# Kernel optimization log

Measured on AMD Instinct MI355X. Metric: run time of the kernel, lower is better.

Reference implementation:

```python
import jax, jax.numpy as jnp
import numpy as np
import math

B, S, H, NH, K = 1, 4096, 1024, 16, 32
HD = H // NH


def setup_inputs() -> dict:
    key = jax.random.key(0)
    ks = jax.random.split(key, 8)
    x = jax.random.normal(ks[0], (B, S, H), dtype=jnp.float32)
    # per-query top-K indices; make them causal (idx[q] <= q) so every row has >=1 valid key
    idx_raw = jax.random.randint(ks[1], (S, K), 0, S)
    idx = idx_raw % (jnp.arange(S)[:, None] + 1)
    valid = jnp.ones((S, K), dtype=bool)
    geo_bias = jax.random.normal(ks[2], (NH, S, K), dtype=jnp.float32)
    scale = 1.0 / math.sqrt(H)
    Wq = jax.random.normal(ks[3], (H, H), dtype=jnp.float32) * scale
    Wk = jax.random.normal(ks[4], (H, H), dtype=jnp.float32) * scale
    Wv = jax.random.normal(ks[5], (H, H), dtype=jnp.float32) * scale
    Wo = jax.random.normal(ks[6], (H, H), dtype=jnp.float32) * scale
    bo = jnp.zeros((H,), dtype=jnp.float32)
    return {"x": x, "idx": idx, "valid": valid, "geo_bias": geo_bias,
            "Wq": Wq, "Wk": Wk, "Wv": Wv, "Wo": Wo, "bo": bo}


def reference(x, idx, valid, geo_bias, Wq, Wk, Wv, Wo, bo):
    b, s, h = x.shape
    nh = geo_bias.shape[0]
    hd = h // nh
    kk = idx.shape[1]
    # projections -> [b, nh, s, hd]
    def proj(W):
        return (x @ W).reshape(b, s, nh, hd).transpose(0, 2, 1, 3)
    q, k, v = proj(Wq), proj(Wk), proj(Wv)
    # gather per-query selected keys/values: [b, nh, s, K, hd]
    k_sel = k[:, :, idx]
    v_sel = v[:, :, idx]
    # scores via elementwise mult + reduce over head_dim
    logits = jnp.einsum('bhsd,bhskd->bhsk', q, k_sel) / math.sqrt(hd)
    logits = logits + geo_bias[None]
    mask = valid & (idx <= jnp.arange(s)[:, None])  # [s, K]
    logits = jnp.where(mask[None, None], logits, jnp.float32(-1e30))
    attn = jax.nn.softmax(logits, axis=-1)
    out = jnp.einsum('bhsk,bhskd->bhsd', attn, v_sel)
    out = out.transpose(0, 2, 1, 3).reshape(b, s, h)
    return out @ Wo + bo
```

## Files before the change

kernel.cpp:

```cpp
#include <hip/hip_runtime.h>
#include <hip/hip_bf16.h>
#include <stdint.h>

typedef unsigned short u16;
typedef __attribute__((ext_vector_type(8))) short bf16x8;
typedef __attribute__((ext_vector_type(4))) float f32x4;
typedef __attribute__((ext_vector_type(2))) float f32x2;

typedef const __attribute__((address_space(1))) unsigned int* gptr_t;
typedef __attribute__((address_space(3))) unsigned int* lptr_t;

__device__ __forceinline__ u16 f2bf(float f) {
    unsigned int u;
    __builtin_memcpy(&u, &f, 4);
    u += 0x7FFFu + ((u >> 16) & 1u);
    return (u16)(u >> 16);
}
__device__ __forceinline__ float bflo(unsigned int u) {
    unsigned int x = u << 16; float f; __builtin_memcpy(&f, &x, 4); return f;
}
__device__ __forceinline__ float bfhi(unsigned int u) {
    unsigned int x = u & 0xFFFF0000u; float f; __builtin_memcpy(&f, &x, 4); return f;
}
__device__ __forceinline__ f32x2 upk(unsigned int u) {
    return (f32x2){bflo(u), bfhi(u)};
}

__global__ __launch_bounds__(256) void gemm_qkv(const u16* __restrict__ A,
                                                const u16* __restrict__ Bt,
                                                u16* __restrict__ C,
                                                int M, int N, int K) {
    __shared__ u16 S[4][4096];

    const int t    = threadIdx.x;
    const int lane = t & 63;
    const int wave = t >> 6;
    const int wm   = (wave >> 1) * 64;
    const int wn   = (wave & 1) * 64;
    const int m0   = blockIdx.y * 128;
    const int n0   = blockIdx.x * 128;

    const int r5   = t >> 2;
    const int pc   = t & 3;
    const int lc   = pc ^ ((r5 >> 1) & 3);

    const int quad = lane >> 4;
    const int l16  = lane & 15;
    const int swz  = (l16 >> 1) & 3;

    const u16* gabase = A  + (size_t)(m0 + r5) * K + lc * 8;
    const u16* gbbase = Bt + (size_t)(n0 + r5) * K + lc * 8;

    f32x4 acc[4][4];
#pragma unroll
    for (int i = 0; i < 4; i++)
#pragma unroll
        for (int j = 0; j < 4; j++) acc[i][j] = (f32x4){0.f, 0.f, 0.f, 0.f};

    const int NT = K >> 5;

#pragma unroll
    for (int p = 0; p < 2; p++) {
        __builtin_amdgcn_global_load_lds((gptr_t)(gabase + (size_t)(64 * p) * K),
                                         (lptr_t)(&S[0][t * 8 + p * 2048]), 16, 0, 0);
        __builtin_amdgcn_global_load_lds((gptr_t)(gbbase + (size_t)(64 * p) * K),
                                         (lptr_t)(&S[2][t * 8 + p * 2048]), 16, 0, 0);
    }
#pragma unroll
    for (int p = 0; p < 2; p++) {
        __builtin_amdgcn_global_load_lds((gptr_t)(gabase + (size_t)(64 * p) * K + 32),
                                         (lptr_t)(&S[1][t * 8 + p * 2048]), 16, 0, 0);
        __builtin_amdgcn_global_load_lds((gptr_t)(gbbase + (size_t)(64 * p) * K + 32),
                                         (lptr_t)(&S[3][t * 8 + p * 2048]), 16, 0, 0);
    }
    asm volatile("s_waitcnt vmcnt(4)");
    __builtin_amdgcn_sched_barrier(0);
    __builtin_amdgcn_s_barrier();

    for (int kt = 0; kt < NT; ++kt) {
        const int buf = kt & 1;

        bf16x8 af[4], bfg[4];
#pragma unroll
        for (int i = 0; i < 4; i++)
            af[i] = *(const bf16x8*)&S[buf][(wm + i * 16 + l16) * 32 + ((quad ^ swz) * 8)];
#pragma unroll
        for (int j = 0; j < 4; j++)
            bfg[j] = *(const bf16x8*)&S[2 + buf][(wn + j * 16 + l16) * 32 + ((quad ^ swz) * 8)];
        asm volatile("s_waitcnt lgkmcnt(0)");
        __builtin_amdgcn_sched_barrier(0);
        __builtin_amdgcn_s_barrier();

        if (kt + 2 < NT) {
            const int k0 = (kt + 2) * 32;
#pragma unroll
            for (int p = 0; p < 2; p++) {
                __builtin_amdgcn_global_load_lds(
                    (gptr_t)(gabase + (size_t)(64 * p) * K + k0),
                    (lptr_t)(&S[buf][t * 8 + p * 2048]), 16, 0, 0);
                __builtin_amdgcn_global_load_lds(
                    (gptr_t)(gbbase + (size_t)(64 * p) * K + k0),
                    (lptr_t)(&S[2 + buf][t * 8 + p * 2048]), 16, 0, 0);
            }
        }

#pragma unroll
        for (int i = 0; i < 4; i++)
#pragma unroll
            for (int j = 0; j < 4; j++)
                acc[i][j] = __builtin_amdgcn_mfma_f32_16x16x32_bf16(af[i], bfg[j], acc[i][j], 0, 0, 0);

        if (kt < NT - 2) {
            asm volatile("s_waitcnt vmcnt(4)");
            __builtin_amdgcn_sched_barrier(0);
            __builtin_amdgcn_s_barrier();
        } else if (kt == NT - 2) {
            asm volatile("s_waitcnt vmcnt(0)");
            __builtin_amdgcn_sched_barrier(0);
            __builtin_amdgcn_s_barrier();
        }
    }

    __syncthreads();

    u16* Cs = &S[0][0];
#pragma unroll
    for (int j = 0; j < 4; j++)
#pragma unroll
        for (int i = 0; i < 4; i++)
#pragma unroll
            for (int r = 0; r < 4; r++)
                Cs[(wm + i * 16 + quad * 4 + r) * 128 + wn + j * 16 + l16] = f2bf(acc[i][j][r]);
    __syncthreads();

#pragma unroll
    for (int p = 0; p < 8; p++) {
        const int row = p * 16 + (t >> 4);
        const int c8  = (t & 15) * 8;
        const uint4 v = *(const uint4*)&Cs[row * 128 + c8];
        *(uint4*)&C[(size_t)(m0 + row) * N + n0 + c8] = v;
    }
}

__global__ __launch_bounds__(256) void gemm_o(const u16* __restrict__ A,
                                              const u16* __restrict__ Bt,
                                              float* __restrict__ C,
                                              const float* __restrict__ bias,
                                              int M, int N, int K) {
    __shared__ u16 As[128 * 64];
    __shared__ u16 Bs[64 * 64];

    const int t    = threadIdx.x;
    const int lane = t & 63;
    const int wave = t >> 6;
    const int wm   = (wave >> 1) * 64;
    const int wn   = (wave & 1) * 32;
    const int m0   = blockIdx.y * 128;
    const int n0   = blockIdx.x * 64;

    const int r5   = t >> 3;
    const int pc   = t & 7;
    const int lc   = pc ^ (r5 & 7);

    const int quad = lane >> 4;
    const int l16  = lane & 15;
    const int sw   = l16 & 7;

    f32x4 acc[4][2];
#pragma unroll
    for (int i = 0; i < 4; i++)
#pragma unroll
        for (int j = 0; j < 2; j++) acc[i][j] = (f32x4){0.f, 0.f, 0.f, 0.f};

    for (int k0 = 0; k0 < K; k0 += 64) {
#pragma unroll
        for (int p = 0; p < 4; p++) {
            const u16* ga = A + (size_t)(m0 + r5 + 32 * p) * K + k0 + lc * 8;
            __builtin_amdgcn_global_load_lds((gptr_t)ga, (lptr_t)(&As[t * 8 + p * 2048]), 16, 0, 0);
        }
#pragma unroll
        for (int p = 0; p < 2; p++) {
            const u16* gb = Bt + (size_t)(n0 + r5 + 32 * p) * K + k0 + lc * 8;
            __builtin_amdgcn_global_load_lds((gptr_t)gb, (lptr_t)(&Bs[t * 8 + p * 2048]), 16, 0, 0);
        }
        __syncthreads();

#pragma unroll
        for (int k2 = 0; k2 < 2; k2++) {
            bf16x8 af[4], bfg[2];
#pragma unroll
            for (int i = 0; i < 4; i++)
                af[i] = *(const bf16x8*)&As[(wm + i * 16 + l16) * 64 + ((k2 * 4 + quad) ^ sw) * 8];
#pragma unroll
            for (int j = 0; j < 2; j++)
                bfg[j] = *(const bf16x8*)&Bs[(wn + j * 16 + l16) * 64 + ((k2 * 4 + quad) ^ sw) * 8];
#pragma unroll
            for (int i = 0; i < 4; i++)
#pragma unroll
                for (int j = 0; j < 2; j++)
                    acc[i][j] = __builtin_amdgcn_mfma_f32_16x16x32_bf16(af[i], bfg[j], acc[i][j], 0, 0, 0);
        }
        __syncthreads();
    }

#pragma unroll
    for (int j = 0; j < 2; j++) {
        const int n  = n0 + wn + j * 16 + l16;
        const float bv = bias ? bias[n] : 0.f;
#pragma unroll
        for (int i = 0; i < 4; i++) {
            const int mbase = m0 + wm + i * 16 + quad * 4;
#pragma unroll
            for (int r = 0; r < 4; r++)
                C[(size_t)(mbase + r) * N + n] = acc[i][j][r] + bv;
        }
    }
}

__global__ __launch_bounds__(256) void prep_k(const float* __restrict__ x,
                                              const float* __restrict__ W0,
                                              const float* __restrict__ W1,
                                              const float* __restrict__ W2,
                                              const float* __restrict__ W3,
                                              u16* __restrict__ x_bf,
                                              u16* __restrict__ Dqkv,
                                              u16* __restrict__ Do) {
    const int b = blockIdx.x;
    if (b < 4096) {
        const int i = b * 256 + threadIdx.x;
        const float4 v = ((const float4*)x)[i];
        u16 o[4] = {f2bf(v.x), f2bf(v.y), f2bf(v.z), f2bf(v.w)};
        *(uint64_t*)&x_bf[i * 4] = *(uint64_t*)o;
        return;
    }
    __shared__ u16 tile[32][33];
    const int bb  = b - 4096;
    const int z   = bb >> 10;
    const int t10 = bb & 1023;
    const int c0  = (t10 & 31) * 32;
    const int r0  = (t10 >> 5) * 32;
    const float* src = (z == 0) ? W0 : (z == 1) ? W1 : (z == 2) ? W2 : W3;
    u16* dst = (z < 3) ? (Dqkv + (size_t)z * 1024 * 1024) : Do;
    const int tx = threadIdx.x & 31;
    const int ty = threadIdx.x >> 5;
#pragma unroll
    for (int i = 0; i < 32; i += 8)
        tile[ty + i][tx] = f2bf(src[(size_t)(r0 + ty + i) * 1024 + c0 + tx]);
    __syncthreads();
#pragma unroll
    for (int i = 0; i < 32; i += 8)
        dst[(size_t)(c0 + ty + i) * 1024 + r0 + tx] = tile[tx][ty + i];
}

__global__ __launch_bounds__(256, 6) void attn_k(const u16* __restrict__ QKV,
                                                 const int* __restrict__ idx,
                                                 const float* __restrict__ geo,
                                                 u16* __restrict__ AO) {
    __shared__ float dot_lds[4 * 64];
    __shared__ float w_lds[4 * 64];

    const int t    = threadIdx.x;
    const int lane = t & 63;
    const int wave = t >> 6;
    const int b    = blockIdx.x;
    const int hp   = b & 7;
    const int s    = ((b >> 3) << 2) + wave;
    const int h0   = hp * 2;
    const int hsel = lane >> 5;
    const int kk   = lane & 31;
    const int g    = lane >> 3;
    const int c8   = lane & 7;

    const char* qb = (const char*)QKV;

    const float gv = geo[((size_t)(h0 + hsel) * 4096 + s) * 32 + kk];
    const int j    = idx[s * 32 + kk];
    const int joff = j * 6144;

    const uint4 qA = *(const uint4*)(qb + (size_t)s * 6144 + h0 * 128 + c8 * 16);
    const uint4 qB = *(const uint4*)(qb + (size_t)s * 6144 + h0 * 128 + 128 + c8 * 16);

    int jsrc0 = __shfl(j, (0 * 8 + g) & 31);
    int jsrc1 = __shfl(j, (1 * 8 + g) & 31);
    int jsrc2 = __shfl(j, (2 * 8 + g) & 31);
    int jsrc3 = __shfl(j, (3 * 8 + g) & 31);

    uint4 kreg[8];
#pragma unroll
    for (int i = 0; i < 8; i++) {
        const int jm = (i & 3) == 0 ? jsrc0 : (i & 3) == 1 ? jsrc1
                     : (i & 3) == 2 ? jsrc2 : jsrc3;
        kreg[i] = *(const uint4*)(qb + (size_t)(unsigned)(jm * 6144) + 2048 +
                                  (h0 + (i >> 2)) * 128 + c8 * 16);
    }
    __builtin_amdgcn_sched_barrier(0);

    const f32x2 qa0 = upk(qA.x), qa1 = upk(qA.y), qa2 = upk(qA.z), qa3 = upk(qA.w);
    const f32x2 qb0 = upk(qB.x), qb1 = upk(qB.y), qb2 = upk(qB.z), qb3 = upk(qB.w);

#pragma unroll
    for (int i = 0; i < 8; i++) {
        const int rh = i * 8 + g;
        f32x2 d2;
        if (i < 4) {
            d2  = upk(kreg[i].x) * qa0;
            d2 += upk(kreg[i].y) * qa1;
            d2 += upk(kreg[i].z) * qa2;
            d2 += upk(kreg[i].w) * qa3;
        } else {
            d2  = upk(kreg[i].x) * qb0;
            d2 += upk(kreg[i].y) * qb1;
            d2 += upk(kreg[i].z) * qb2;
            d2 += upk(kreg[i].w) * qb3;
        }
        float d = d2.x + d2.y;
        d += __shfl_xor(d, 1);
        d += __shfl_xor(d, 2);
        d += __shfl_xor(d, 4);
        if (c8 == 0) dot_lds[wave * 64 + rh] = d;
    }

    float lg2 = dot_lds[wave * 64 + lane] * 0.125f + gv;
    if (j > s) lg2 = -1e30f;
    lg2 = fminf(lg2, 80.f);

    const float p = __expf(lg2);
    float sum = p;
    sum += __shfl_xor(sum, 16);
    sum += __shfl_xor(sum, 8);
    sum += __shfl_xor(sum, 4);
    sum += __shfl_xor(sum, 2);
    sum += __shfl_xor(sum, 1);
    const float w = p / sum;
    w_lds[wave * 64 + lane] = w;

    const int half = lane >> 5;
    const int e8   = lane & 31;
    const int vconst = 4096 + h0 * 128 + 8 * e8;
    uint2 vreg[16];
#pragma unroll
    for (int i = 0; i < 16; i++) {
        const int jo = __shfl(joff, 2 * i + half);
        vreg[i] = *(const uint2*)(qb + (size_t)(unsigned)jo + vconst);
    }
    __builtin_amdgcn_sched_barrier(0);

    const int whead = (e8 >> 4) * 32;
    f32x2 a01a = (f32x2){0.f, 0.f}, a01b = (f32x2){0.f, 0.f};
    f32x2 a23a = (f32x2){0.f, 0.f}, a23b = (f32x2){0.f, 0.f};
#pragma unroll
    for (int i = 0; i < 16; i += 2) {
        const float w0 = w_lds[wave * 64 + whead + 2 * i + half];
        const float w1 = w_lds[wave * 64 + whead + 2 * (i + 1) + half];
        a01a += w0 * upk(vreg[i].x);
        a23a += w0 * upk(vreg[i].y);
        a01b += w1 * upk(vreg[i + 1].x);
        a23b += w1 * upk(vreg[i + 1].y);
    }
    f32x2 av01 = a01a + a01b;
    f32x2 av23 = a23a + a23b;
    av01.x += __shfl_xor(av01.x, 32);
    av01.y += __shfl_xor(av01.y, 32);
    av23.x += __shfl_xor(av23.x, 32);
    av23.y += __shfl_xor(av23.y, 32);
    if (lane < 32) {
        u16 o[4] = {f2bf(av01.x), f2bf(av01.y), f2bf(av23.x), f2bf(av23.y)};
        *(uint2*)&AO[(size_t)s * 1024 + h0 * 64 + 4 * lane] = *(uint2*)o;
    }
}

extern "C" void kernel_launch(void* const* d_in, const int* in_sizes, int n_in,
                              void* d_out, int out_size, void* d_ws, size_t ws_size,
                              hipStream_t stream) {
    const float* x   = (const float*)d_in[0];
    const int*   idx = (const int*)d_in[1];
    const float* geo = (const float*)d_in[3];
    const float* Wq  = (const float*)d_in[4];
    const float* Wk  = (const float*)d_in[5];
    const float* Wv  = (const float*)d_in[6];
    const float* Wo  = (const float*)d_in[7];
    const float* bo  = (const float*)d_in[8];
    float* out = (float*)d_out;

    u16* x_bf   = (u16*)d_ws;
    u16* wt_qkv = x_bf + (size_t)4096 * 1024;
    u16* wt_o   = wt_qkv + (size_t)3 * 1024 * 1024;
    u16* qkv    = wt_o + (size_t)1024 * 1024;
    u16* ao     = qkv + (size_t)4096 * 3072;

    const dim3 tb(256);
    prep_k<<<dim3(8192), tb, 0, stream>>>(x, Wq, Wk, Wv, Wo, x_bf, wt_qkv, wt_o);

    gemm_qkv<<<dim3(3072 / 128, 4096 / 128), tb, 0, stream>>>(
        x_bf, wt_qkv, qkv, 4096, 3072, 1024);
    attn_k<<<dim3(4096 * 8 / 4), tb, 0, stream>>>(qkv, idx, geo, ao);
    gemm_o<<<dim3(1024 / 64, 4096 / 128), tb, 0, stream>>>(
        ao, wt_o, out, bo, 4096, 1024, 1024);
}
```

Baseline: 182.0 us.

## Remap QK dot lanes to 4-lane groups and load V indices directly

```diff
diff --git a/kernel.cpp b/kernel.cpp
--- a/kernel.cpp
+++ b/kernel.cpp
@@ -268,56 +268,64 @@
     const int h0   = hp * 2;
     const int hsel = lane >> 5;
     const int kk   = lane & 31;
-    const int g    = lane >> 3;
-    const int c8   = lane & 7;
+    const int c4   = lane & 3;
+    const int g16  = lane >> 2;
 
     const char* qb = (const char*)QKV;
 
     const float gv = geo[((size_t)(h0 + hsel) * 4096 + s) * 32 + kk];
     const int j    = idx[s * 32 + kk];
-    const int joff = j * 6144;
-
-    const uint4 qA = *(const uint4*)(qb + (size_t)s * 6144 + h0 * 128 + c8 * 16);
-    const uint4 qB = *(const uint4*)(qb + (size_t)s * 6144 + h0 * 128 + 128 + c8 * 16);
-
-    int jsrc0 = __shfl(j, (0 * 8 + g) & 31);
-    int jsrc1 = __shfl(j, (1 * 8 + g) & 31);
-    int jsrc2 = __shfl(j, (2 * 8 + g) & 31);
-    int jsrc3 = __shfl(j, (3 * 8 + g) & 31);
-
-    uint4 kreg[8];
-#pragma unroll
-    for (int i = 0; i < 8; i++) {
-        const int jm = (i & 3) == 0 ? jsrc0 : (i & 3) == 1 ? jsrc1
-                     : (i & 3) == 2 ? jsrc2 : jsrc3;
-        kreg[i] = *(const uint4*)(qb + (size_t)(unsigned)(jm * 6144) + 2048 +
-                                  (h0 + (i >> 2)) * 128 + c8 * 16);
-    }
-    __builtin_amdgcn_sched_barrier(0);
-
-    const f32x2 qa0 = upk(qA.x), qa1 = upk(qA.y), qa2 = upk(qA.z), qa3 = upk(qA.w);
-    const f32x2 qb0 = upk(qB.x), qb1 = upk(qB.y), qb2 = upk(qB.z), qb3 = upk(qB.w);
-
-#pragma unroll
-    for (int i = 0; i < 8; i++) {
-        const int rh = i * 8 + g;
+
+    const int jA = idx[s * 32 + g16];
+    const int jB = idx[s * 32 + 16 + g16];
+
+    const int half = lane >> 5;
+    const uint4 jv0 = *(const uint4*)&idx[s * 32 + 16 * half + 0];
+    const uint4 jv1 = *(const uint4*)&idx[s * 32 + 16 * half + 4];
+    const uint4 jv2 = *(const uint4*)&idx[s * 32 + 16 * half + 8];
+    const uint4 jv3 = *(const uint4*)&idx[s * 32 + 16 * half + 12];
+    const int jvs[16] = {(int)jv0.x, (int)jv0.y, (int)jv0.z, (int)jv0.w,
+                         (int)jv1.x, (int)jv1.y, (int)jv1.z, (int)jv1.w,
+                         (int)jv2.x, (int)jv2.y, (int)jv2.z, (int)jv2.w,
+                         (int)jv3.x, (int)jv3.y, (int)jv3.z, (int)jv3.w};
+
+    const char* qrow = qb + (size_t)s * 6144 + h0 * 128;
+    const uint4 qA0 = *(const uint4*)(qrow + c4 * 16);
+    const uint4 qA1 = *(const uint4*)(qrow + 64 + c4 * 16);
+    const uint4 qB0 = *(const uint4*)(qrow + 128 + c4 * 16);
+    const uint4 qB1 = *(const uint4*)(qrow + 192 + c4 * 16);
+
+#pragma unroll
+    for (int i = 0; i < 4; i++) {
+        const int ji = (i & 1) ? jB : jA;
+        const char* kb = qb + (size_t)(unsigned)(ji * 6144) + 2048 +
+                         (h0 + (i >> 1)) * 128;
+        const uint4 k0 = *(const uint4*)(kb + c4 * 16);
+        const uint4 k1 = *(const uint4*)(kb + 64 + c4 * 16);
         f32x2 d2;
-        if (i < 4) {
-            d2  = upk(kreg[i].x) * qa0;
-            d2 += upk(kreg[i].y) * qa1;
-            d2 += upk(kreg[i].z) * qa2;
-            d2 += upk(kreg[i].w) * qa3;
+        if (i < 2) {
+            d2  = upk(k0.x) * upk(qA0.x);
+            d2 += upk(k0.y) * upk(qA0.y);
+            d2 += upk(k0.z) * upk(qA0.z);
+            d2 += upk(k0.w) * upk(qA0.w);
+            d2 += upk(k1.x) * upk(qA1.x);
+            d2 += upk(k1.y) * upk(qA1.y);
+            d2 += upk(k1.z) * upk(qA1.z);
+            d2 += upk(k1.w) * upk(qA1.w);
         } else {
-            d2  = upk(kreg[i].x) * qb0;
-            d2 += upk(kreg[i].y) * qb1;
-            d2 += upk(kreg[i].z) * qb2;
-            d2 += upk(kreg[i].w) * qb3;
+            d2  = upk(k0.x) * upk(qB0.x);
+            d2 += upk(k0.y) * upk(qB0.y);
+            d2 += upk(k0.z) * upk(qB0.z);
+            d2 += upk(k0.w) * upk(qB0.w);
+            d2 += upk(k1.x) * upk(qB1.x);
+            d2 += upk(k1.y) * upk(qB1.y);
+            d2 += upk(k1.z) * upk(qB1.z);
+            d2 += upk(k1.w) * upk(qB1.w);
         }
         float d = d2.x + d2.y;
         d += __shfl_xor(d, 1);
         d += __shfl_xor(d, 2);
-        d += __shfl_xor(d, 4);
-        if (c8 == 0) dot_lds[wave * 64 + rh] = d;
+        if (c4 == 0) dot_lds[wave * 64 + i * 16 + g16] = d;
     }
 
     float lg2 = dot_lds[wave * 64 + lane] * 0.125f + gv;
@@ -334,28 +342,22 @@
     const float w = p / sum;
     w_lds[wave * 64 + lane] = w;
 
-    const int half = lane >> 5;
     const int e8   = lane & 31;
     const int vconst = 4096 + h0 * 128 + 8 * e8;
-    uint2 vreg[16];
-#pragma unroll
-    for (int i = 0; i < 16; i++) {
-        const int jo = __shfl(joff, 2 * i + half);
-        vreg[i] = *(const uint2*)(qb + (size_t)(unsigned)jo + vconst);
-    }
-    __builtin_amdgcn_sched_barrier(0);
-
-    const int whead = (e8 >> 4) * 32;
+    const int whead  = (e8 >> 4) * 32;
+    const int wbase  = wave * 64 + whead + 16 * half;
     f32x2 a01a = (f32x2){0.f, 0.f}, a01b = (f32x2){0.f, 0.f};
     f32x2 a23a = (f32x2){0.f, 0.f}, a23b = (f32x2){0.f, 0.f};
 #pragma unroll
     for (int i = 0; i < 16; i += 2) {
-        const float w0 = w_lds[wave * 64 + whead + 2 * i + half];
-        const float w1 = w_lds[wave * 64 + whead + 2 * (i + 1) + half];
-        a01a += w0 * upk(vreg[i].x);
-        a23a += w0 * upk(vreg[i].y);
-        a01b += w1 * upk(vreg[i + 1].x);
-        a23b += w1 * upk(vreg[i + 1].y);
+        const float w0 = w_lds[wbase + i];
+        const float w1 = w_lds[wbase + i + 1];
+        const uint2 v0 = *(const uint2*)(qb + (size_t)(unsigned)(jvs[i] * 6144) + vconst);
+        const uint2 v1 = *(const uint2*)(qb + (size_t)(unsigned)(jvs[i + 1] * 6144) + vconst);
+        a01a += w0 * upk(v0.x);
+        a23a += w0 * upk(v0.y);
+        a01b += w1 * upk(v1.x);
+        a23b += w1 * upk(v1.y);
     }
     f32x2 av01 = a01a + a01b;
     f32x2 av23 = a23a + a23b;
```

New measurement: 187.0 us. +2.7%, slower.
